# Optimization experiments

Measured on AMD Instinct MI355X. Metric: run time of the kernel, lower is better.

The kernel has to match this reference:

```python
import jax, jax.numpy as jnp
import numpy as np
from functools import partial

ZONEOUT = 0.1  # eval-mode zoneout: h = h_new + zr*(h_prev - h_new)


def gru_layer(x, h0, kernel, recurrent, bias, zr):
    """Keras v2 GRU (reset_after=True), gate order [z, r, h].
    x: [B,T,D], h0: [B,U], kernel: [D,3U], recurrent: [U,3U], bias: [2,3U].
    Returns pre-zoneout outputs [B,T,U]; zoneout applies only to the carried state."""
    U = h0.shape[-1]
    b_in, b_rec = bias[0], bias[1]
    # precompute input projection for all timesteps (the compute-heavy GEMM)
    xw = jnp.einsum('btd,dk->btk', x, kernel) + b_in  # [B,T,3U]

    def step(h, xw_t):
        m = h @ recurrent + b_rec                      # [B,3U]
        xz, xr, xh = xw_t[:, :U], xw_t[:, U:2 * U], xw_t[:, 2 * U:]
        mz, mr, mh = m[:, :U], m[:, U:2 * U], m[:, 2 * U:]
        z = jax.nn.sigmoid(xz + mz)
        r = jax.nn.sigmoid(xr + mr)
        hh = jnp.tanh(xh + r * mh)
        h_new = z * h + (1.0 - z) * hh                 # cell output
        h_carry = h_new + zr * (h - h_new)             # eval zoneout on state
        return h_carry, h_new

    _, ys = jax.lax.scan(step, h0, jnp.swapaxes(xw, 0, 1))  # scan over T
    return jnp.swapaxes(ys, 0, 1)  # [B,T,U]


def setup_inputs() -> dict:
    key = jax.random.key(0)
    ks = jax.random.split(key, 16)
    B, T, D, U = 32, 1024, 256, 512
    s_in, s_rec = 1.0 / np.sqrt(D), 1.0 / np.sqrt(U)
    return {
        'x':   jax.random.normal(ks[0], (B, T, D), jnp.float32),
        'k0':  jax.random.normal(ks[1], (D, 3 * U), jnp.float32) * s_in,
        'r0':  jax.random.normal(ks[2], (U, 3 * U), jnp.float32) * s_rec,
        'b0':  jnp.zeros((2, 3 * U), jnp.float32),
        'ks':  jax.random.normal(ks[3], (U, 3 * U), jnp.float32) * s_rec,
        'rs':  jax.random.normal(ks[4], (U, 3 * U), jnp.float32) * s_rec,
        'bs':  jnp.zeros((2, 3 * U), jnp.float32),
        'h00': jax.random.normal(ks[5], (1, U), jnp.float32),
        'h01': jax.random.normal(ks[6], (1, U), jnp.float32),
        'h02': jax.random.normal(ks[7], (1, U), jnp.float32),
        'a':   jnp.ones((3,), jnp.float32),  # scalar skip multipliers a_11, a_12, a_22
        'wd':  jax.random.normal(ks[8], (U, D), jnp.float32) * s_rec,
        'bd':  jnp.zeros((D,), jnp.float32),
    }


def reference(x, k0, r0, b0, ks, rs, bs, h00, h01, h02, a, wd, bd):
    B = x.shape[0]
    tile = lambda h: jnp.tile(h, (B, 1))  # learnable init state -> batch
    # layer 0
    out0 = gru_layer(x, tile(h00), k0, r0, b0, ZONEOUT)
    # RK-style skip connections with a SHARED cell but per-layer learnable init states
    h0_skip = [tile(h01), tile(h02)]
    intermediates = []
    x_cur = out0
    idx = 0
    for i in range(2):  # num_skip_connections = num_rnn_layers - 1 = 2
        pred = gru_layer(x_cur, h0_skip[i], ks, rs, bs, ZONEOUT)
        intermediates.append(pred)
        x_cur = out0
        for j in range(i + 1):
            x_cur = x_cur + a[idx] * intermediates[j]
            idx += 1
    # dense output head (linear)
    return jnp.einsum('btu,ud->btd', x_cur, wd) + bd
```

## Files before the change

kernel.cpp:

```cpp
#include <hip/hip_runtime.h>

typedef __attribute__((ext_vector_type(8))) short short8;
typedef __attribute__((ext_vector_type(4))) float f32x4;
typedef __attribute__((ext_vector_type(4))) unsigned short u16x4;
typedef unsigned short ushort;
typedef unsigned long long ull;

#define MFMA16(a,b,c) __builtin_amdgcn_mfma_f32_16x16x32_bf16((a),(b),(c),0,0,0)

static __device__ __forceinline__ float bf2f(ushort u){
  union { unsigned int i; float f; } z; z.i = ((unsigned int)u) << 16; return z.f;
}
static __device__ __forceinline__ ushort f2bf(float f){
  union { float f; unsigned int i; } z; z.f = f;
  unsigned int x = z.i;
  unsigned int r = (x + 0x7fffu + ((x >> 16) & 1u)) >> 16;
  return (ushort)r;
}

static __device__ __forceinline__ short8 ld_hc16(const ushort* p){
  union { ull q[2]; short8 v; } u;
  u.q[0] = __hip_atomic_load((const ull*)p, __ATOMIC_RELAXED, __HIP_MEMORY_SCOPE_AGENT);
  u.q[1] = __hip_atomic_load((const ull*)(p + 4), __ATOMIC_RELAXED, __HIP_MEMORY_SCOPE_AGENT);
  return u.v;
}
static __device__ __forceinline__ float ld_ring_bf(const ushort* base, int idx){
  const unsigned int* p = (const unsigned int*)(base + (idx & ~1));
  unsigned int w = __hip_atomic_load(p, __ATOMIC_RELAXED, __HIP_MEMORY_SCOPE_AGENT);
  return bf2f((idx & 1) ? (ushort)(w >> 16) : (ushort)(w & 0xffffu));
}
static __device__ __forceinline__ void st_hc2(ushort* p, ushort v){
  unsigned int vv = v;
  asm volatile("global_store_short %0, %1, off sc0 sc1" :: "v"(p), "v"(vv) : "memory");
}
static __device__ __forceinline__ void st_hc8(ushort* p, ull v){
  asm volatile("global_store_dwordx2 %0, %1, off sc0 sc1" :: "v"(p), "v"(v) : "memory");
}

static __device__ __forceinline__ void ld_frag16(const ushort* p, short8* o){
  asm volatile(
    "global_load_dwordx4 %0, %16, off sc0 sc1\n\t"
    "global_load_dwordx4 %1, %16, off offset:64 sc0 sc1\n\t"
    "global_load_dwordx4 %2, %16, off offset:128 sc0 sc1\n\t"
    "global_load_dwordx4 %3, %16, off offset:192 sc0 sc1\n\t"
    "global_load_dwordx4 %4, %16, off offset:256 sc0 sc1\n\t"
    "global_load_dwordx4 %5, %16, off offset:320 sc0 sc1\n\t"
    "global_load_dwordx4 %6, %16, off offset:384 sc0 sc1\n\t"
    "global_load_dwordx4 %7, %16, off offset:448 sc0 sc1\n\t"
    "global_load_dwordx4 %8, %16, off offset:512 sc0 sc1\n\t"
    "global_load_dwordx4 %9, %16, off offset:576 sc0 sc1\n\t"
    "global_load_dwordx4 %10, %16, off offset:640 sc0 sc1\n\t"
    "global_load_dwordx4 %11, %16, off offset:704 sc0 sc1\n\t"
    "global_load_dwordx4 %12, %16, off offset:768 sc0 sc1\n\t"
    "global_load_dwordx4 %13, %16, off offset:832 sc0 sc1\n\t"
    "global_load_dwordx4 %14, %16, off offset:896 sc0 sc1\n\t"
    "global_load_dwordx4 %15, %16, off offset:960 sc0 sc1\n\t"
    "s_waitcnt vmcnt(0)"
    : "=&v"(o[0]), "=&v"(o[1]), "=&v"(o[2]), "=&v"(o[3]),
      "=&v"(o[4]), "=&v"(o[5]), "=&v"(o[6]), "=&v"(o[7]),
      "=&v"(o[8]), "=&v"(o[9]), "=&v"(o[10]), "=&v"(o[11]),
      "=&v"(o[12]), "=&v"(o[13]), "=&v"(o[14]), "=&v"(o[15])
    : "v"(p)
    : "memory");
  __builtin_amdgcn_sched_barrier(0);
}

__global__ __launch_bounds__(256) void cvt_k(
    const float* __restrict__ in, ushort* __restrict__ out, int n)
{
  int i = (blockIdx.x * 256 + threadIdx.x) * 4;
  if (i < n){
    float4 v = *(const float4*)(in + i);
    u16x4 o = { f2bf(v.x), f2bf(v.y), f2bf(v.z), f2bf(v.w) };
    *(u16x4*)(out + i) = o;
  }
}

template<int F32OUT>
__global__ __launch_bounds__(256) void gemm_bias_k(
    const ushort* __restrict__ A,
    const ushort* __restrict__ B,
    const float*  __restrict__ bias,
    void* __restrict__ Cv,
    int M, int N, int K)
{
  __shared__ __align__(16) ushort Blds[64 * 40];
  const int tid  = threadIdx.x;
  const int wid  = tid >> 6;
  const int lane = tid & 63;
  const int quad = lane >> 4;
  const int lc   = lane & 15;
  const int nb   = N >> 6;
  const int bn   = (blockIdx.x % nb) << 6;
  const int bm   = (blockIdx.x / nb) << 6;

  const int sk  = tid >> 3;
  const int scg = tid & 7;

  f32x4 acc[4] = {{0,0,0,0},{0,0,0,0},{0,0,0,0},{0,0,0,0}};
  const int arow = bm + wid * 16 + lc;
  const ushort* aptr = A + (size_t)arow * K + quad * 8;

  for (int k0 = 0; k0 < K; k0 += 32){
    short8 bv = *(const short8*)(B + (size_t)(k0 + sk) * N + bn + (scg << 3));
    #pragma unroll
    for (int i = 0; i < 8; ++i){
      int c = (scg << 3) + i;
      int p = c * 40 + (((sk >> 3) ^ (scg & 3)) << 3) + (sk & 7);
      Blds[p] = (ushort)bv[i];
    }
    __syncthreads();
    short8 av = *(const short8*)(aptr + k0);
    #pragma unroll
    for (int nt = 0; nt < 4; ++nt){
      int c2 = (nt << 4) + lc;
      int p  = c2 * 40 + ((quad ^ ((c2 >> 3) & 3)) << 3);
      short8 bfrag = *(const short8*)(Blds + p);
      acc[nt] = MFMA16(av, bfrag, acc[nt]);
    }
    __syncthreads();
  }
  #pragma unroll
  for (int nt = 0; nt < 4; ++nt){
    #pragma unroll
    for (int i = 0; i < 4; ++i){
      int m = bm + wid * 16 + quad * 4 + i;
      int n = bn + (nt << 4) + lc;
      float v = acc[nt][i] + bias[n];
      if (F32OUT) ((float*)Cv)[(size_t)m * N + n] = v;
      else        ((ushort*)Cv)[(size_t)m * N + n] = f2bf(v);
    }
  }
}

#define NWG 96
#define RD 8
#define FSTEPS 1032

__global__ __launch_bounds__(384, 1) void rec3_k(
    const ushort* __restrict__ xw0,
    const ushort* __restrict__ R0b,
    const ushort* __restrict__ Ksb,
    const ushort* __restrict__ Rsb,
    const float*  __restrict__ b0v,
    const float*  __restrict__ bsv,
    const float*  __restrict__ h00,
    const float*  __restrict__ h01,
    const float*  __restrict__ h02,
    const float*  __restrict__ av,
    ushort* __restrict__ comb,
    ushort* __restrict__ rings,
    int* __restrict__ flags)
{
  __shared__ float m_lds[3][32][17];
  __shared__ float x_lds[3][32][17];
  __shared__ float bias_l[96];
  __shared__ __align__(16) ushort ks_lds[3 * 16 * 64 * 8];

  const int tid  = threadIdx.x;
  const int wid  = tid >> 6;
  const int lane = tid & 63;
  const int quad = lane >> 4;
  const int lc   = lane & 15;
  const int bid  = blockIdx.x;
  const int role = bid >> 5;
  const int g    = bid & 31;
  const int ug0  = g << 4;
  const int gate = wid % 3, mtile = wid / 3;
  const int col0 = (gate << 9) + ug0;

  ushort* h_ring    = rings + role * 131072;
  ushort* out0ring  = rings + 393216;
  ushort* pred0ring = rings + 524288;
  ushort* xw1ring   = rings + 655360;

  const ushort* Rw = (role == 0) ? R0b : Rsb;
  short8 bfragR[16];
  #pragma unroll
  for (int f = 0; f < 16; ++f){
    short8 v;
    #pragma unroll
    for (int j = 0; j < 8; ++j)
      v[j] = (short)Rw[(size_t)(f * 32 + quad * 8 + j) * 1536 + col0 + lc];
    bfragR[f] = v;
  }
  if (role > 0 && mtile == 0){
    #pragma unroll
    for (int f = 0; f < 16; ++f){
      short8 v;
      #pragma unroll
      for (int j = 0; j < 8; ++j)
        v[j] = (short)Ksb[(size_t)(f * 32 + quad * 8 + j) * 1536 + col0 + lc];
      *(short8*)(ks_lds + (((gate << 4) + f) << 9) + (lane << 3)) = v;
    }
  }
  const float* brec = ((role == 0) ? b0v : bsv) + 1536;
  if (tid < 48) bias_l[tid] = brec[(tid >> 4) * 512 + ug0 + (tid & 15)];
  if (tid >= 48 && tid < 96) bias_l[tid] = bsv[((tid - 48) >> 4) * 512 + ug0 + ((tid - 48) & 15)];
  const float a0 = av[0], a1 = av[1], a2 = av[2];
  const float* hinit = (role == 0) ? h00 : (role == 1) ? h01 : h02;

  const int  b0i  = tid >> 4;
  const int  u0   = tid & 15;
  const int  b1i  = (tid + 384) >> 4;
  const bool has1 = (tid < 128);
  const int  uu   = ug0 + u0;
  float hp0 = hinit[uu];
  float hp1 = hp0;

  ushort xz0 = 0, xr0 = 0, xh0 = 0, xz1 = 0, xr1 = 0, xh1 = 0;
  if (role == 0){
    size_t r0_ = ((size_t)b0i * 1024) * 1536 + uu;
    xz0 = xw0[r0_]; xr0 = xw0[r0_ + 512]; xh0 = xw0[r0_ + 1024];
    if (has1){
      size_t r1_ = ((size_t)b1i * 1024) * 1536 + uu;
      xz1 = xw0[r1_]; xr1 = xw0[r1_ + 512]; xh1 = xw0[r1_ + 1024];
    }
  }
  __syncthreads();

  long budget = 40000000L;
  for (int t = 0; t < 1024; ++t){
    const int s     = t + role;
    const int slot  = t & (RD - 1);
    const int pslot = (t - 1) & (RD - 1);

    ushort nz0 = 0, nr0 = 0, nh0 = 0, nz1 = 0, nr1 = 0, nh1 = 0;
    if (role == 0 && t < 1023){
      size_t r0_ = ((size_t)b0i * 1024 + t + 1) * 1536 + uu;
      nz0 = xw0[r0_]; nr0 = xw0[r0_ + 512]; nh0 = xw0[r0_ + 1024];
      if (has1){
        size_t r1_ = ((size_t)b1i * 1024 + t + 1) * 1536 + uu;
        nz1 = xw0[r1_]; nr1 = xw0[r1_ + 512]; nh1 = xw0[r1_ + 1024];
      }
    }

    {
      const bool needO = (t > 0);
      const bool needP = (role >= 1);
      const bool needF = (role <= 1) && (s >= RD);
      if ((needO || needP || needF) && wid == 0){
        const int  l    = lane & 31;
        const int* fo   = flags + (role * FSTEPS + (s - 1)) * 32 + l;
        const int* fp   = flags + ((role - 1) * FSTEPS + (s - 1)) * 32 + l;
        const int* ff   = flags + (2 * FSTEPS + (s - 6)) * 32 + l;
        while (budget > 0){
          bool ok = true;
          if (needO) ok &= (__hip_atomic_load(fo, __ATOMIC_RELAXED, __HIP_MEMORY_SCOPE_AGENT) != 0);
          if (needP) ok &= (__hip_atomic_load(fp, __ATOMIC_RELAXED, __HIP_MEMORY_SCOPE_AGENT) != 0);
          if (needF) ok &= (__hip_atomic_load(ff, __ATOMIC_RELAXED, __HIP_MEMORY_SCOPE_AGENT) != 0);
          if (__ballot(ok) == ~0ull) break;
          --budget;
        }
      }
      __syncthreads();
    }

    float o_s0 = 0, p_s0 = 0, x1z0 = 0, x1r0 = 0, x1h0 = 0;
    float o_s1 = 0, p_s1 = 0, x1z1 = 0, x1r1 = 0, x1h1 = 0;
    if (role == 2){
      int rb0 = slot * 16384 + b0i * 512 + uu;
      o_s0 = ld_ring_bf(out0ring, rb0);
      p_s0 = ld_ring_bf(pred0ring, rb0);
      ull xwp = __hip_atomic_load((const ull*)(xw1ring + (size_t)((slot * 32 + b0i) * 512 + uu) * 4),
                                  __ATOMIC_RELAXED, __HIP_MEMORY_SCOPE_AGENT);
      x1z0 = bf2f((ushort)(xwp & 0xffffu));
      x1r0 = bf2f((ushort)((xwp >> 16) & 0xffffu));
      x1h0 = bf2f((ushort)((xwp >> 32) & 0xffffu));
      if (has1){
        int rb1 = slot * 16384 + b1i * 512 + uu;
        o_s1 = ld_ring_bf(out0ring, rb1);
        p_s1 = ld_ring_bf(pred0ring, rb1);
        ull xwq = __hip_atomic_load((const ull*)(xw1ring + (size_t)((slot * 32 + b1i) * 512 + uu) * 4),
                                    __ATOMIC_RELAXED, __HIP_MEMORY_SCOPE_AGENT);
        x1z1 = bf2f((ushort)(xwq & 0xffffu));
        x1r1 = bf2f((ushort)((xwq >> 16) & 0xffffu));
        x1h1 = bf2f((ushort)((xwq >> 32) & 0xffffu));
      }
    }

    {
      short8 avm[16];
      short8 avx[16];
      if (role >= 1){
        const ushort* xr_ = ((role == 1) ? out0ring : pred0ring)
                          + slot * 16384 + (mtile * 16 + lc) * 512 + quad * 8;
        ld_frag16(xr_, avx);
      }
      if (t == 0){
        #pragma unroll
        for (int f = 0; f < 16; ++f){
          short8 v;
          #pragma unroll
          for (int j = 0; j < 8; ++j)
            v[j] = (short)f2bf(hinit[f * 32 + quad * 8 + j]);
          avm[f] = v;
        }
      } else {
        const ushort* hr = h_ring + pslot * 16384 + (mtile * 16 + lc) * 512 + quad * 8;
        ld_frag16(hr, avm);
      }

      f32x4 am0 = {0,0,0,0}, am1 = {0,0,0,0};
      if (role == 0){
        #pragma unroll
        for (int f = 0; f < 16; ++f){
          if (f & 1) am1 = MFMA16(avm[f], bfragR[f], am1);
          else       am0 = MFMA16(avm[f], bfragR[f], am0);
        }
        f32x4 am = am0 + am1;
        #pragma unroll
        for (int i = 0; i < 4; ++i)
          m_lds[gate][(mtile << 4) + (quad << 2) + i][lc] = am[i];
      } else {
        f32x4 ax0 = {0,0,0,0}, ax1 = {0,0,0,0};
        #pragma unroll
        for (int f = 0; f < 16; ++f){
          short8 bx = *(const short8*)(ks_lds + (((gate << 4) + f) << 9) + (lane << 3));
          if (f & 1){ am1 = MFMA16(avm[f], bfragR[f], am1); ax1 = MFMA16(avx[f], bx, ax1); }
          else      { am0 = MFMA16(avm[f], bfragR[f], am0); ax0 = MFMA16(avx[f], bx, ax0); }
        }
        f32x4 am = am0 + am1, ax = ax0 + ax1;
        #pragma unroll
        for (int i = 0; i < 4; ++i){
          m_lds[gate][(mtile << 4) + (quad << 2) + i][lc] = am[i];
          x_lds[gate][(mtile << 4) + (quad << 2) + i][lc] = ax[i];
        }
      }
    }
    __syncthreads();

    ushort cb0 = 0, cb1 = 0;
    {
      int b = b0i;
      float mz = m_lds[0][b][u0] + bias_l[u0];
      float mr = m_lds[1][b][u0] + bias_l[16 + u0];
      float mh = m_lds[2][b][u0] + bias_l[32 + u0];
      float xz, xr, xh;
      if (role == 0){ xz = bf2f(xz0); xr = bf2f(xr0); xh = bf2f(xh0); }
      else if (role == 1){
        xz = x_lds[0][b][u0] + bias_l[48 + u0];
        xr = x_lds[1][b][u0] + bias_l[64 + u0];
        xh = x_lds[2][b][u0] + bias_l[80 + u0];
      } else {
        xz = x1z0 + a0 * x_lds[0][b][u0] + bias_l[48 + u0];
        xr = x1r0 + a0 * x_lds[1][b][u0] + bias_l[64 + u0];
        xh = x1h0 + a0 * x_lds[2][b][u0] + bias_l[80 + u0];
      }
      float z  = 1.f / (1.f + __expf(-(xz + mz)));
      float r  = 1.f / (1.f + __expf(-(xr + mr)));
      float axv = xh + r * mh;
      float hh = 1.f - 2.f / (1.f + __expf(2.f * axv));
      float hn = z * hp0 + (1.f - z) * hh;
      float hcv = hn + 0.1f * (hp0 - hn);
      hp0 = hcv;
      int rb = slot * 16384 + b * 512 + uu;
      st_hc2(h_ring + rb, f2bf(hcv));
      if (role == 0) st_hc2(out0ring + rb, f2bf(hn));
      else if (role == 1){
        st_hc2(pred0ring + rb, f2bf(hn));
        ull pv = (ull)f2bf(x_lds[0][b][u0])
               | ((ull)f2bf(x_lds[1][b][u0]) << 16)
               | ((ull)f2bf(x_lds[2][b][u0]) << 32);
        st_hc8(xw1ring + (size_t)((slot * 32 + b) * 512 + uu) * 4, pv);
      } else {
        cb0 = f2bf(o_s0 + a1 * p_s0 + a2 * hn);
      }
    }
    if (has1){
      int b = b1i;
      float mz = m_lds[0][b][u0] + bias_l[u0];
      float mr = m_lds[1][b][u0] + bias_l[16 + u0];
      float mh = m_lds[2][b][u0] + bias_l[32 + u0];
      float xz, xr, xh;
      if (role == 0){ xz = bf2f(xz1); xr = bf2f(xr1); xh = bf2f(xh1); }
      else if (role == 1){
        xz = x_lds[0][b][u0] + bias_l[48 + u0];
        xr = x_lds[1][b][u0] + bias_l[64 + u0];
        xh = x_lds[2][b][u0] + bias_l[80 + u0];
      } else {
        xz = x1z1 + a0 * x_lds[0][b][u0] + bias_l[48 + u0];
        xr = x1r1 + a0 * x_lds[1][b][u0] + bias_l[64 + u0];
        xh = x1h1 + a0 * x_lds[2][b][u0] + bias_l[80 + u0];
      }
      float z  = 1.f / (1.f + __expf(-(xz + mz)));
      float r  = 1.f / (1.f + __expf(-(xr + mr)));
      float axv = xh + r * mh;
      float hh = 1.f - 2.f / (1.f + __expf(2.f * axv));
      float hn = z * hp1 + (1.f - z) * hh;
      float hcv = hn + 0.1f * (hp1 - hn);
      hp1 = hcv;
      int rb = slot * 16384 + b * 512 + uu;
      st_hc2(h_ring + rb, f2bf(hcv));
      if (role == 0) st_hc2(out0ring + rb, f2bf(hn));
      else if (role == 1){
        st_hc2(pred0ring + rb, f2bf(hn));
        ull pv = (ull)f2bf(x_lds[0][b][u0])
               | ((ull)f2bf(x_lds[1][b][u0]) << 16)
               | ((ull)f2bf(x_lds[2][b][u0]) << 32);
        st_hc8(xw1ring + (size_t)((slot * 32 + b) * 512 + uu) * 4, pv);
      } else {
        cb1 = f2bf(o_s1 + a1 * p_s1 + a2 * hn);
      }
    }
    asm volatile("s_waitcnt vmcnt(0)" ::: "memory");
    __syncthreads();
    if (tid == 0)
      __hip_atomic_store(flags + (role * FSTEPS + s) * 32 + g, 1,
                         __ATOMIC_RELAXED, __HIP_MEMORY_SCOPE_AGENT);
    if (role == 2){
      comb[((size_t)b0i * 1024 + t) * 512 + uu] = cb0;
      if (has1) comb[((size_t)b1i * 1024 + t) * 512 + uu] = cb1;
    }

    if (role == 0){
      xz0 = nz0; xr0 = nr0; xh0 = nh0;
      xz1 = nz1; xr1 = nr1; xh1 = nh1;
    }
  }
}

extern "C" void kernel_launch(void* const* d_in, const int* in_sizes, int n_in,
                              void* d_out, int out_size, void* d_ws, size_t ws_size,
                              hipStream_t stream)
{
  const float* x   = (const float*)d_in[0];
  const float* k0  = (const float*)d_in[1];
  const float* r0  = (const float*)d_in[2];
  const float* b0  = (const float*)d_in[3];
  const float* ks  = (const float*)d_in[4];
  const float* rs  = (const float*)d_in[5];
  const float* bs  = (const float*)d_in[6];
  const float* h00 = (const float*)d_in[7];
  const float* h01 = (const float*)d_in[8];
  const float* h02 = (const float*)d_in[9];
  const float* a   = (const float*)d_in[10];
  const float* wd  = (const float*)d_in[11];
  const float* bd  = (const float*)d_in[12];
  float* outp = (float*)d_out;

  char* ws = (char*)d_ws;
  ushort* XW    = (ushort*)(ws);
  ushort* combp = (ushort*)(ws + 100663296u);
  ushort* xbf   = combp;
  ushort* rings = (ushort*)(ws + 134217728u);
  int*    flags = (int*)   (ws + 136577024u);
  ushort* k0b   = (ushort*)(ws + 136973312u);
  ushort* r0b   = (ushort*)(ws + 137759744u);
  ushort* ksb   = (ushort*)(ws + 139332608u);
  ushort* rsb   = (ushort*)(ws + 140905472u);
  ushort* wdb   = (ushort*)(ws + 142478336u);

  hipMemsetAsync(flags, 0, 3 * FSTEPS * 32 * sizeof(int), stream);

  dim3 blk(256);
  cvt_k<<<dim3(8192), blk, 0, stream>>>(x,  xbf, 8388608);
  cvt_k<<<dim3(384),  blk, 0, stream>>>(k0, k0b, 393216);
  cvt_k<<<dim3(768),  blk, 0, stream>>>(r0, r0b, 786432);
  cvt_k<<<dim3(768),  blk, 0, stream>>>(ks, ksb, 786432);
  cvt_k<<<dim3(768),  blk, 0, stream>>>(rs, rsb, 786432);
  cvt_k<<<dim3(128),  blk, 0, stream>>>(wd, wdb, 131072);

  gemm_bias_k<0><<<dim3(512 * 24), blk, 0, stream>>>(xbf, k0b, b0, XW, 32768, 1536, 256);
  rec3_k<<<dim3(NWG), dim3(384), 0, stream>>>(XW, r0b, ksb, rsb, b0, bs,
                                              h00, h01, h02, a, combp, rings, flags);
  gemm_bias_k<1><<<dim3(512 * 4), blk, 0, stream>>>(combp, wdb, bd, outp, 32768, 256, 512);
}
```

Measured before the change: 10.65 ms.

## Replace per-step flag barriers with tagged ring entries and double-buffered LDS

Each bf16 value written to the inter-workgroup rings now carries a 16-bit step tag in the same dword, so consumers spin directly on the data until the tag matches instead of waiting on separate per-step flags. This removes the wait-for-stores fence, the trailing __syncthreads and the flag-polling phase on every recurrent step, and adds double-buffered m/x LDS tiles so the next step's writes cannot overwrite data still being read. Only the role-2 backpressure flag remains, and the skip-cell recurrent weights move from registers to LDS. The cost is twice the ring traffic and more polling of payload lines, plus some risk from the 16-bit tag and the reduced h ring depth of 2.

```diff
diff --git a/kernel.cpp b/kernel.cpp
--- a/kernel.cpp
+++ b/kernel.cpp
@@ -3,6 +3,7 @@
 typedef __attribute__((ext_vector_type(8))) short short8;
 typedef __attribute__((ext_vector_type(4))) float f32x4;
 typedef __attribute__((ext_vector_type(4))) unsigned short u16x4;
+typedef __attribute__((ext_vector_type(4))) unsigned int u32x4;
 typedef unsigned short ushort;
 typedef unsigned long long ull;
 
@@ -18,51 +19,66 @@
   return (ushort)r;
 }
 
-static __device__ __forceinline__ short8 ld_hc16(const ushort* p){
-  union { ull q[2]; short8 v; } u;
-  u.q[0] = __hip_atomic_load((const ull*)p, __ATOMIC_RELAXED, __HIP_MEMORY_SCOPE_AGENT);
-  u.q[1] = __hip_atomic_load((const ull*)(p + 4), __ATOMIC_RELAXED, __HIP_MEMORY_SCOPE_AGENT);
-  return u.v;
-}
-static __device__ __forceinline__ float ld_ring_bf(const ushort* base, int idx){
-  const unsigned int* p = (const unsigned int*)(base + (idx & ~1));
-  unsigned int w = __hip_atomic_load(p, __ATOMIC_RELAXED, __HIP_MEMORY_SCOPE_AGENT);
-  return bf2f((idx & 1) ? (ushort)(w >> 16) : (ushort)(w & 0xffffu));
-}
-static __device__ __forceinline__ void st_hc2(ushort* p, ushort v){
-  unsigned int vv = v;
-  asm volatile("global_store_short %0, %1, off sc0 sc1" :: "v"(p), "v"(vv) : "memory");
-}
-static __device__ __forceinline__ void st_hc8(ushort* p, ull v){
+static __device__ __forceinline__ void st_hc4(unsigned int* p, unsigned int v){
+  asm volatile("global_store_dword %0, %1, off sc0 sc1" :: "v"(p), "v"(v) : "memory");
+}
+static __device__ __forceinline__ void st_hc8q(ull* p, ull v){
   asm volatile("global_store_dwordx2 %0, %1, off sc0 sc1" :: "v"(p), "v"(v) : "memory");
 }
 
-static __device__ __forceinline__ void ld_frag16(const ushort* p, short8* o){
+static __device__ __forceinline__ void ld_tag16(const unsigned int* p, u32x4* w){
   asm volatile(
     "global_load_dwordx4 %0, %16, off sc0 sc1\n\t"
-    "global_load_dwordx4 %1, %16, off offset:64 sc0 sc1\n\t"
+    "global_load_dwordx4 %1, %16, off offset:16 sc0 sc1\n\t"
     "global_load_dwordx4 %2, %16, off offset:128 sc0 sc1\n\t"
-    "global_load_dwordx4 %3, %16, off offset:192 sc0 sc1\n\t"
+    "global_load_dwordx4 %3, %16, off offset:144 sc0 sc1\n\t"
     "global_load_dwordx4 %4, %16, off offset:256 sc0 sc1\n\t"
-    "global_load_dwordx4 %5, %16, off offset:320 sc0 sc1\n\t"
+    "global_load_dwordx4 %5, %16, off offset:272 sc0 sc1\n\t"
     "global_load_dwordx4 %6, %16, off offset:384 sc0 sc1\n\t"
-    "global_load_dwordx4 %7, %16, off offset:448 sc0 sc1\n\t"
+    "global_load_dwordx4 %7, %16, off offset:400 sc0 sc1\n\t"
     "global_load_dwordx4 %8, %16, off offset:512 sc0 sc1\n\t"
-    "global_load_dwordx4 %9, %16, off offset:576 sc0 sc1\n\t"
+    "global_load_dwordx4 %9, %16, off offset:528 sc0 sc1\n\t"
     "global_load_dwordx4 %10, %16, off offset:640 sc0 sc1\n\t"
-    "global_load_dwordx4 %11, %16, off offset:704 sc0 sc1\n\t"
+    "global_load_dwordx4 %11, %16, off offset:656 sc0 sc1\n\t"
     "global_load_dwordx4 %12, %16, off offset:768 sc0 sc1\n\t"
-    "global_load_dwordx4 %13, %16, off offset:832 sc0 sc1\n\t"
+    "global_load_dwordx4 %13, %16, off offset:784 sc0 sc1\n\t"
     "global_load_dwordx4 %14, %16, off offset:896 sc0 sc1\n\t"
-    "global_load_dwordx4 %15, %16, off offset:960 sc0 sc1\n\t"
+    "global_load_dwordx4 %15, %16, off offset:912 sc0 sc1\n\t"
     "s_waitcnt vmcnt(0)"
-    : "=&v"(o[0]), "=&v"(o[1]), "=&v"(o[2]), "=&v"(o[3]),
-      "=&v"(o[4]), "=&v"(o[5]), "=&v"(o[6]), "=&v"(o[7]),
-      "=&v"(o[8]), "=&v"(o[9]), "=&v"(o[10]), "=&v"(o[11]),
-      "=&v"(o[12]), "=&v"(o[13]), "=&v"(o[14]), "=&v"(o[15])
+    : "=&v"(w[0]), "=&v"(w[1]), "=&v"(w[2]), "=&v"(w[3]),
+      "=&v"(w[4]), "=&v"(w[5]), "=&v"(w[6]), "=&v"(w[7]),
+      "=&v"(w[8]), "=&v"(w[9]), "=&v"(w[10]), "=&v"(w[11]),
+      "=&v"(w[12]), "=&v"(w[13]), "=&v"(w[14]), "=&v"(w[15])
     : "v"(p)
     : "memory");
   __builtin_amdgcn_sched_barrier(0);
+}
+
+static __device__ __forceinline__ void load_tagged8(
+    const unsigned int* p, unsigned int tag, short8* dst, long& budget)
+{
+  u32x4 w[16];
+  for (;;){
+    ld_tag16(p, w);
+    bool ok = true;
+    #pragma unroll
+    for (int i = 0; i < 16; ++i){
+      ok = ok & ((w[i].x & 0xffffu) == tag) & ((w[i].y & 0xffffu) == tag)
+              & ((w[i].z & 0xffffu) == tag) & ((w[i].w & 0xffffu) == tag);
+    }
+    if (__ballot(ok) == ~0ull) break;
+    budget -= 16;
+    if (budget <= 0) break;
+  }
+  #pragma unroll
+  for (int f = 0; f < 8; ++f){
+    short8 v;
+    v[0] = (short)(w[2*f].x >> 16);   v[1] = (short)(w[2*f].y >> 16);
+    v[2] = (short)(w[2*f].z >> 16);   v[3] = (short)(w[2*f].w >> 16);
+    v[4] = (short)(w[2*f+1].x >> 16); v[5] = (short)(w[2*f+1].y >> 16);
+    v[6] = (short)(w[2*f+1].z >> 16); v[7] = (short)(w[2*f+1].w >> 16);
+    dst[f] = v;
+  }
 }
 
 __global__ __launch_bounds__(256) void cvt_k(
@@ -134,8 +150,7 @@
 }
 
 #define NWG 96
-#define RD 8
-#define FSTEPS 1032
+#define RD8 8
 
 __global__ __launch_bounds__(384, 1) void rec3_k(
     const ushort* __restrict__ xw0,
@@ -149,13 +164,14 @@
     const float*  __restrict__ h02,
     const float*  __restrict__ av,
     ushort* __restrict__ comb,
-    ushort* __restrict__ rings,
-    int* __restrict__ flags)
+    unsigned int* __restrict__ rings4,
+    int* __restrict__ flags2)
 {
-  __shared__ float m_lds[3][32][17];
-  __shared__ float x_lds[3][32][17];
+  __shared__ float m_lds[2][3][32][17];
+  __shared__ float x_lds[2][3][32][17];
   __shared__ float bias_l[96];
   __shared__ __align__(16) ushort ks_lds[3 * 16 * 64 * 8];
+  __shared__ __align__(16) ushort rs_lds[3 * 16 * 64 * 8];
 
   const int tid  = threadIdx.x;
   const int wid  = tid >> 6;
@@ -169,29 +185,41 @@
   const int gate = wid % 3, mtile = wid / 3;
   const int col0 = (gate << 9) + ug0;
 
-  ushort* h_ring    = rings + role * 131072;
-  ushort* out0ring  = rings + 393216;
-  ushort* pred0ring = rings + 524288;
-  ushort* xw1ring   = rings + 655360;
-
-  const ushort* Rw = (role == 0) ? R0b : Rsb;
+  unsigned int* h_ring4    = rings4 + role * 32768;
+  unsigned int* out0ring4  = rings4 + 98304;
+  unsigned int* pred0ring4 = rings4 + 229376;
+  ull*          xw1q       = (ull*)(rings4 + 360448);
+
   short8 bfragR[16];
-  #pragma unroll
-  for (int f = 0; f < 16; ++f){
-    short8 v;
-    #pragma unroll
-    for (int j = 0; j < 8; ++j)
-      v[j] = (short)Rw[(size_t)(f * 32 + quad * 8 + j) * 1536 + col0 + lc];
-    bfragR[f] = v;
-  }
-  if (role > 0 && mtile == 0){
+  if (role == 0){
     #pragma unroll
     for (int f = 0; f < 16; ++f){
       short8 v;
       #pragma unroll
       for (int j = 0; j < 8; ++j)
-        v[j] = (short)Ksb[(size_t)(f * 32 + quad * 8 + j) * 1536 + col0 + lc];
-      *(short8*)(ks_lds + (((gate << 4) + f) << 9) + (lane << 3)) = v;
+        v[j] = (short)R0b[(size_t)(f * 32 + quad * 8 + j) * 1536 + col0 + lc];
+      bfragR[f] = v;
+    }
+  }
+  if (role > 0){
+    if (mtile == 0){
+      #pragma unroll
+      for (int f = 0; f < 16; ++f){
+        short8 v;
+        #pragma unroll
+        for (int j = 0; j < 8; ++j)
+          v[j] = (short)Ksb[(size_t)(f * 32 + quad * 8 + j) * 1536 + col0 + lc];
+        *(short8*)(ks_lds + (((gate << 4) + f) << 9) + (lane << 3)) = v;
+      }
+    } else {
+      #pragma unroll
+      for (int f = 0; f < 16; ++f){
+        short8 v;
+        #pragma unroll
+        for (int j = 0; j < 8; ++j)
+          v[j] = (short)Rsb[(size_t)(f * 32 + quad * 8 + j) * 1536 + col0 + lc];
+        *(short8*)(rs_lds + (((gate << 4) + f) << 9) + (lane << 3)) = v;
+      }
     }
   }
   const float* brec = ((role == 0) ? b0v : bsv) + 1536;
@@ -221,9 +249,13 @@
 
   long budget = 40000000L;
   for (int t = 0; t < 1024; ++t){
-    const int s     = t + role;
-    const int slot  = t & (RD - 1);
-    const int pslot = (t - 1) & (RD - 1);
+    const int s      = t + role;
+    const int slot8  = t & (RD8 - 1);
+    const int slot2  = t & 1;
+    const int pslot2 = (t - 1) & 1;
+    const int par    = t & 1;
+    const unsigned int tagH = (unsigned int)t;
+    const unsigned int tagX = (unsigned int)(t + 1);
 
     ushort nz0 = 0, nr0 = 0, nh0 = 0, nz1 = 0, nr1 = 0, nh1 = 0;
     if (role == 0 && t < 1023){
@@ -235,57 +267,64 @@
       }
     }
 
-    {
-      const bool needO = (t > 0);
-      const bool needP = (role >= 1);
-      const bool needF = (role <= 1) && (s >= RD);
-      if ((needO || needP || needF) && wid == 0){
-        const int  l    = lane & 31;
-        const int* fo   = flags + (role * FSTEPS + (s - 1)) * 32 + l;
-        const int* fp   = flags + ((role - 1) * FSTEPS + (s - 1)) * 32 + l;
-        const int* ff   = flags + (2 * FSTEPS + (s - 6)) * 32 + l;
-        while (budget > 0){
-          bool ok = true;
-          if (needO) ok &= (__hip_atomic_load(fo, __ATOMIC_RELAXED, __HIP_MEMORY_SCOPE_AGENT) != 0);
-          if (needP) ok &= (__hip_atomic_load(fp, __ATOMIC_RELAXED, __HIP_MEMORY_SCOPE_AGENT) != 0);
-          if (needF) ok &= (__hip_atomic_load(ff, __ATOMIC_RELAXED, __HIP_MEMORY_SCOPE_AGENT) != 0);
-          if (__ballot(ok) == ~0ull) break;
-          --budget;
-        }
-      }
-      __syncthreads();
+    if (role <= 1 && s >= RD8){
+      const int* ff = flags2 + ((s - 6) & 63) * 32 + (lane & 31);
+      while (budget > 0){
+        bool ok = (__hip_atomic_load(ff, __ATOMIC_RELAXED, __HIP_MEMORY_SCOPE_AGENT) >= s - 5);
+        if (__ballot(ok) == ~0ull) break;
+        --budget;
+      }
     }
 
     float o_s0 = 0, p_s0 = 0, x1z0 = 0, x1r0 = 0, x1h0 = 0;
     float o_s1 = 0, p_s1 = 0, x1z1 = 0, x1r1 = 0, x1h1 = 0;
-    if (role == 2){
-      int rb0 = slot * 16384 + b0i * 512 + uu;
-      o_s0 = ld_ring_bf(out0ring, rb0);
-      p_s0 = ld_ring_bf(pred0ring, rb0);
-      ull xwp = __hip_atomic_load((const ull*)(xw1ring + (size_t)((slot * 32 + b0i) * 512 + uu) * 4),
-                                  __ATOMIC_RELAXED, __HIP_MEMORY_SCOPE_AGENT);
-      x1z0 = bf2f((ushort)(xwp & 0xffffu));
-      x1r0 = bf2f((ushort)((xwp >> 16) & 0xffffu));
-      x1h0 = bf2f((ushort)((xwp >> 32) & 0xffffu));
-      if (has1){
-        int rb1 = slot * 16384 + b1i * 512 + uu;
-        o_s1 = ld_ring_bf(out0ring, rb1);
-        p_s1 = ld_ring_bf(pred0ring, rb1);
-        ull xwq = __hip_atomic_load((const ull*)(xw1ring + (size_t)((slot * 32 + b1i) * 512 + uu) * 4),
-                                    __ATOMIC_RELAXED, __HIP_MEMORY_SCOPE_AGENT);
-        x1z1 = bf2f((ushort)(xwq & 0xffffu));
-        x1r1 = bf2f((ushort)((xwq >> 16) & 0xffffu));
-        x1h1 = bf2f((ushort)((xwq >> 32) & 0xffffu));
-      }
-    }
-
+    short8 avm[16];
+    short8 avx[16];
     {
-      short8 avm[16];
-      short8 avx[16];
+      const int rowoff = (mtile * 16 + lc) * 512 + quad * 8;
       if (role >= 1){
-        const ushort* xr_ = ((role == 1) ? out0ring : pred0ring)
-                          + slot * 16384 + (mtile * 16 + lc) * 512 + quad * 8;
-        ld_frag16(xr_, avx);
+        const unsigned int* xr_ = ((role == 1) ? out0ring4 : pred0ring4)
+                                + slot8 * 16384 + rowoff;
+        load_tagged8(xr_,       tagX, avx,     budget);
+        load_tagged8(xr_ + 256, tagX, avx + 8, budget);
+      }
+      if (role == 2){
+        const unsigned int* o0p = out0ring4  + slot8 * 16384 + b0i * 512 + uu;
+        const unsigned int* p0p = pred0ring4 + slot8 * 16384 + b0i * 512 + uu;
+        const ull* x0p = xw1q + (size_t)(slot8 * 32 + b0i) * 512 + uu;
+        const unsigned int* o1p = out0ring4  + slot8 * 16384 + b1i * 512 + uu;
+        const unsigned int* p1p = pred0ring4 + slot8 * 16384 + b1i * 512 + uu;
+        const ull* x1p = xw1q + (size_t)(slot8 * 32 + b1i) * 512 + uu;
+        unsigned int ow0, pw0, ow1 = 0, pw1 = 0; ull xq0, xq1 = 0;
+        for (;;){
+          ow0 = __hip_atomic_load(o0p, __ATOMIC_RELAXED, __HIP_MEMORY_SCOPE_AGENT);
+          pw0 = __hip_atomic_load(p0p, __ATOMIC_RELAXED, __HIP_MEMORY_SCOPE_AGENT);
+          xq0 = __hip_atomic_load(x0p, __ATOMIC_RELAXED, __HIP_MEMORY_SCOPE_AGENT);
+          bool ok = ((ow0 & 0xffffu) == tagX) & ((pw0 & 0xffffu) == tagX)
+                  & ((unsigned int)(xq0 & 0xffffull) == tagX);
+          if (has1){
+            ow1 = __hip_atomic_load(o1p, __ATOMIC_RELAXED, __HIP_MEMORY_SCOPE_AGENT);
+            pw1 = __hip_atomic_load(p1p, __ATOMIC_RELAXED, __HIP_MEMORY_SCOPE_AGENT);
+            xq1 = __hip_atomic_load(x1p, __ATOMIC_RELAXED, __HIP_MEMORY_SCOPE_AGENT);
+            ok = ok & ((ow1 & 0xffffu) == tagX) & ((pw1 & 0xffffu) == tagX)
+                    & ((unsigned int)(xq1 & 0xffffull) == tagX);
+          }
+          if (__ballot(ok) == ~0ull) break;
+          budget -= 6;
+          if (budget <= 0) break;
+        }
+        o_s0 = bf2f((ushort)(ow0 >> 16));
+        p_s0 = bf2f((ushort)(pw0 >> 16));
+        x1z0 = bf2f((ushort)(xq0 >> 48));
+        x1r0 = bf2f((ushort)((xq0 >> 32) & 0xffffull));
+        x1h0 = bf2f((ushort)((xq0 >> 16) & 0xffffull));
+        if (has1){
+          o_s1 = bf2f((ushort)(ow1 >> 16));
+          p_s1 = bf2f((ushort)(pw1 >> 16));
+          x1z1 = bf2f((ushort)(xq1 >> 48));
+          x1r1 = bf2f((ushort)((xq1 >> 32) & 0xffffull));
+          x1h1 = bf2f((ushort)((xq1 >> 16) & 0xffffull));
+        }
       }
       if (t == 0){
         #pragma unroll
@@ -297,10 +336,13 @@
           avm[f] = v;
         }
       } else {
-        const ushort* hr = h_ring + pslot * 16384 + (mtile * 16 + lc) * 512 + quad * 8;
-        ld_frag16(hr, avm);
-      }
-
+        const unsigned int* hr = h_ring4 + pslot2 * 16384 + rowoff;
+        load_tagged8(hr,       tagH, avm,     budget);
+        load_tagged8(hr + 256, tagH, avm + 8, budget);
+      }
+    }
+
+    {
       f32x4 am0 = {0,0,0,0}, am1 = {0,0,0,0};
       if (role == 0){
         #pragma unroll
@@ -311,41 +353,46 @@
         f32x4 am = am0 + am1;
         #pragma unroll
         for (int i = 0; i < 4; ++i)
-          m_lds[gate][(mtile << 4) + (quad << 2) + i][lc] = am[i];
+          m_lds[par][gate][(mtile << 4) + (quad << 2) + i][lc] = am[i];
       } else {
         f32x4 ax0 = {0,0,0,0}, ax1 = {0,0,0,0};
         #pragma unroll
         for (int f = 0; f < 16; ++f){
           short8 bx = *(const short8*)(ks_lds + (((gate << 4) + f) << 9) + (lane << 3));
-          if (f & 1){ am1 = MFMA16(avm[f], bfragR[f], am1); ax1 = MFMA16(avx[f], bx, ax1); }
-          else      { am0 = MFMA16(avm[f], bfragR[f], am0); ax0 = MFMA16(avx[f], bx, ax0); }
+          short8 br = *(const short8*)(rs_lds + (((gate << 4) + f) << 9) + (lane << 3));
+          if (f & 1){ am1 = MFMA16(avm[f], br, am1); ax1 = MFMA16(avx[f], bx, ax1); }
+          else      { am0 = MFMA16(avm[f], br, am0); ax0 = MFMA16(avx[f], bx, ax0); }
         }
         f32x4 am = am0 + am1, ax = ax0 + ax1;
         #pragma unroll
         for (int i = 0; i < 4; ++i){
-          m_lds[gate][(mtile << 4) + (quad << 2) + i][lc] = am[i];
-          x_lds[gate][(mtile << 4) + (quad << 2) + i][lc] = ax[i];
+          m_lds[par][gate][(mtile << 4) + (quad << 2) + i][lc] = am[i];
+          x_lds[par][gate][(mtile << 4) + (quad << 2) + i][lc] = ax[i];
         }
       }
     }
     __syncthreads();
+
+    if (role == 2 && tid == 0)
+      __hip_atomic_store(flags2 + (s & 63) * 32 + g, s + 1,
+                         __ATOMIC_RELAXED, __HIP_MEMORY_SCOPE_AGENT);
 
     ushort cb0 = 0, cb1 = 0;
     {
       int b = b0i;
-      float mz = m_lds[0][b][u0] + bias_l[u0];
-      float mr = m_lds[1][b][u0] + bias_l[16 + u0];
-      float mh = m_lds[2][b][u0] + bias_l[32 + u0];
+      float mz = m_lds[par][0][b][u0] + bias_l[u0];
+      float mr = m_lds[par][1][b][u0] + bias_l[16 + u0];
+      float mh = m_lds[par][2][b][u0] + bias_l[32 + u0];
       float xz, xr, xh;
       if (role == 0){ xz = bf2f(xz0); xr = bf2f(xr0); xh = bf2f(xh0); }
       else if (role == 1){
-        xz = x_lds[0][b][u0] + bias_l[48 + u0];
-        xr = x_lds[1][b][u0] + bias_l[64 + u0];
-        xh = x_lds[2][b][u0] + bias_l[80 + u0];
+        xz = x_lds[par][0][b][u0] + bias_l[48 + u0];
+        xr = x_lds[par][1][b][u0] + bias_l[64 + u0];
+        xh = x_lds[par][2][b][u0] + bias_l[80 + u0];
       } else {
-        xz = x1z0 + a0 * x_lds[0][b][u0] + bias_l[48 + u0];
-        xr = x1r0 + a0 * x_lds[1][b][u0] + bias_l[64 + u0];
-        xh = x1h0 + a0 * x_lds[2][b][u0] + bias_l[80 + u0];
+        xz = x1z0 + a0 * x_lds[par][0][b][u0] + bias_l[48 + u0];
+        xr = x1r0 + a0 * x_lds[par][1][b][u0] + bias_l[64 + u0];
+        xh = x1h0 + a0 * x_lds[par][2][b][u0] + bias_l[80 + u0];
       }
       float z  = 1.f / (1.f + __expf(-(xz + mz)));
       float r  = 1.f / (1.f + __expf(-(xr + mr)));
@@ -354,34 +401,38 @@
       float hn = z * hp0 + (1.f - z) * hh;
       float hcv = hn + 0.1f * (hp0 - hn);
       hp0 = hcv;
-      int rb = slot * 16384 + b * 512 + uu;
-      st_hc2(h_ring + rb, f2bf(hcv));
-      if (role == 0) st_hc2(out0ring + rb, f2bf(hn));
-      else if (role == 1){
-        st_hc2(pred0ring + rb, f2bf(hn));
-        ull pv = (ull)f2bf(x_lds[0][b][u0])
-               | ((ull)f2bf(x_lds[1][b][u0]) << 16)
-               | ((ull)f2bf(x_lds[2][b][u0]) << 32);
-        st_hc8(xw1ring + (size_t)((slot * 32 + b) * 512 + uu) * 4, pv);
+      unsigned int tg = (unsigned int)(t + 1);
+      st_hc4(h_ring4 + slot2 * 16384 + b * 512 + uu,
+             ((unsigned int)f2bf(hcv) << 16) | tg);
+      if (role == 0){
+        st_hc4(out0ring4 + slot8 * 16384 + b * 512 + uu,
+               ((unsigned int)f2bf(hn) << 16) | tg);
+      } else if (role == 1){
+        st_hc4(pred0ring4 + slot8 * 16384 + b * 512 + uu,
+               ((unsigned int)f2bf(hn) << 16) | tg);
+        ull pv = ((ull)f2bf(x_lds[par][0][b][u0]) << 48)
+               | ((ull)f2bf(x_lds[par][1][b][u0]) << 32)
+               | ((ull)f2bf(x_lds[par][2][b][u0]) << 16) | (ull)tg;
+        st_hc8q(xw1q + (size_t)(slot8 * 32 + b) * 512 + uu, pv);
       } else {
         cb0 = f2bf(o_s0 + a1 * p_s0 + a2 * hn);
       }
     }
     if (has1){
       int b = b1i;
-      float mz = m_lds[0][b][u0] + bias_l[u0];
-      float mr = m_lds[1][b][u0] + bias_l[16 + u0];
-      float mh = m_lds[2][b][u0] + bias_l[32 + u0];
+      float mz = m_lds[par][0][b][u0] + bias_l[u0];
+      float mr = m_lds[par][1][b][u0] + bias_l[16 + u0];
+      float mh = m_lds[par][2][b][u0] + bias_l[32 + u0];
       float xz, xr, xh;
       if (role == 0){ xz = bf2f(xz1); xr = bf2f(xr1); xh = bf2f(xh1); }
       else if (role == 1){
-        xz = x_lds[0][b][u0] + bias_l[48 + u0];
-        xr = x_lds[1][b][u0] + bias_l[64 + u0];
-        xh = x_lds[2][b][u0] + bias_l[80 + u0];
+        xz = x_lds[par][0][b][u0] + bias_l[48 + u0];
+        xr = x_lds[par][1][b][u0] + bias_l[64 + u0];
+        xh = x_lds[par][2][b][u0] + bias_l[80 + u0];
       } else {
-        xz = x1z1 + a0 * x_lds[0][b][u0] + bias_l[48 + u0];
-        xr = x1r1 + a0 * x_lds[1][b][u0] + bias_l[64 + u0];
-        xh = x1h1 + a0 * x_lds[2][b][u0] + bias_l[80 + u0];
+        xz = x1z1 + a0 * x_lds[par][0][b][u0] + bias_l[48 + u0];
+        xr = x1r1 + a0 * x_lds[par][1][b][u0] + bias_l[64 + u0];
+        xh = x1h1 + a0 * x_lds[par][2][b][u0] + bias_l[80 + u0];
       }
       float z  = 1.f / (1.f + __expf(-(xz + mz)));
       float r  = 1.f / (1.f + __expf(-(xr + mr)));
@@ -390,24 +441,23 @@
       float hn = z * hp1 + (1.f - z) * hh;
       float hcv = hn + 0.1f * (hp1 - hn);
       hp1 = hcv;
-      int rb = slot * 16384 + b * 512 + uu;
-      st_hc2(h_ring + rb, f2bf(hcv));
-      if (role == 0) st_hc2(out0ring + rb, f2bf(hn));
-      else if (role == 1){
-        st_hc2(pred0ring + rb, f2bf(hn));
-        ull pv = (ull)f2bf(x_lds[0][b][u0])
-               | ((ull)f2bf(x_lds[1][b][u0]) << 16)
-               | ((ull)f2bf(x_lds[2][b][u0]) << 32);
-        st_hc8(xw1ring + (size_t)((slot * 32 + b) * 512 + uu) * 4, pv);
+      unsigned int tg = (unsigned int)(t + 1);
+      st_hc4(h_ring4 + slot2 * 16384 + b * 512 + uu,
+             ((unsigned int)f2bf(hcv) << 16) | tg);
+      if (role == 0){
+        st_hc4(out0ring4 + slot8 * 16384 + b * 512 + uu,
+               ((unsigned int)f2bf(hn) << 16) | tg);
+      } else if (role == 1){
+        st_hc4(pred0ring4 + slot8 * 16384 + b * 512 + uu,
+               ((unsigned int)f2bf(hn) << 16) | tg);
+        ull pv = ((ull)f2bf(x_lds[par][0][b][u0]) << 48)
+               | ((ull)f2bf(x_lds[par][1][b][u0]) << 32)
+               | ((ull)f2bf(x_lds[par][2][b][u0]) << 16) | (ull)tg;
+        st_hc8q(xw1q + (size_t)(slot8 * 32 + b) * 512 + uu, pv);
       } else {
         cb1 = f2bf(o_s1 + a1 * p_s1 + a2 * hn);
       }
     }
-    asm volatile("s_waitcnt vmcnt(0)" ::: "memory");
-    __syncthreads();
-    if (tid == 0)
-      __hip_atomic_store(flags + (role * FSTEPS + s) * 32 + g, 1,
-                         __ATOMIC_RELAXED, __HIP_MEMORY_SCOPE_AGENT);
     if (role == 2){
       comb[((size_t)b0i * 1024 + t) * 512 + uu] = cb0;
       if (has1) comb[((size_t)b1i * 1024 + t) * 512 + uu] = cb1;
@@ -443,15 +493,15 @@
   ushort* XW    = (ushort*)(ws);
   ushort* combp = (ushort*)(ws + 100663296u);
   ushort* xbf   = combp;
-  ushort* rings = (ushort*)(ws + 134217728u);
-  int*    flags = (int*)   (ws + 136577024u);
+  unsigned int* rings4 = (unsigned int*)(ws + 134217728u);
+  int*    flags2 = (int*)(ws + 134217728u + 2490368u);
   ushort* k0b   = (ushort*)(ws + 136973312u);
   ushort* r0b   = (ushort*)(ws + 137759744u);
   ushort* ksb   = (ushort*)(ws + 139332608u);
   ushort* rsb   = (ushort*)(ws + 140905472u);
   ushort* wdb   = (ushort*)(ws + 142478336u);
 
-  hipMemsetAsync(flags, 0, 3 * FSTEPS * 32 * sizeof(int), stream);
+  hipMemsetAsync(rings4, 0, 2490368u + 8192u, stream);
 
   dim3 blk(256);
   cvt_k<<<dim3(8192), blk, 0, stream>>>(x,  xbf, 8388608);
@@ -463,6 +513,6 @@
 
   gemm_bias_k<0><<<dim3(512 * 24), blk, 0, stream>>>(xbf, k0b, b0, XW, 32768, 1536, 256);
   rec3_k<<<dim3(NWG), dim3(384), 0, stream>>>(XW, r0b, ksb, rsb, b0, bs,
-                                              h00, h01, h02, a, combp, rings, flags);
+                                              h00, h01, h02, a, combp, rings4, flags2);
   gemm_bias_k<1><<<dim3(512 * 4), blk, 0, stream>>>(combp, wdb, bd, outp, 32768, 256, 512);
 }
```

New measurement: 15.53 ms. 45.9% more time.
